# Performance work log

Hardware: AMD Instinct MI355X
Metric: run time of the kernel (lower is better)

The kernel has to match this reference:

```python
import jax, jax.numpy as jnp
import numpy as np

EPS_PD = 1e-6      # torch.nn.PairwiseDistance default eps (added to the difference)
EPS_NORM = 1e-12   # F.normalize default eps

B, D, C = 1024, 512, 256  # batch, in_features, out_features


def _l2_normalize(x, axis):
    n = jnp.linalg.norm(x, axis=axis, keepdims=True)
    return x / jnp.maximum(n, EPS_NORM)


def _pairwise_dist(a, b):
    # Faithful to torch PairwiseDistance(p=2) with the unsqueeze(2)/t().unsqueeze(0)
    # broadcast trick: norm over the feature dim of (a[:, :, None] - b.T[None, :, :] + eps).
    # a: [N, D], b: [M, D] -> [N, M]
    diff = a[:, :, None] - b.T[None, :, :] + EPS_PD  # [N, D, M]
    return jnp.sqrt(jnp.sum(diff * diff, axis=1))


def setup_inputs() -> dict:
    key = jax.random.key(0)
    k1, k2, k3 = jax.random.split(key, 3)
    return {
        "features": jax.random.normal(k1, (B, D), dtype=jnp.float32),
        "weights": jax.random.normal(k2, (C, D), dtype=jnp.float32),          # nn.init.normal_(0,1)
        "distance_scale": jax.random.normal(k3, (1,), dtype=jnp.float32),
        "use_distance_scale": 1,
    }


def reference(features, weights, distance_scale, use_distance_scale):
    f = _l2_normalize(features, axis=1)   # [B, D]
    w = _l2_normalize(weights, axis=1)    # [C, D]
    distances = _pairwise_dist(f, w)          # [B, C]
    distances_protoc = _pairwise_dist(w, w)   # [C, C]
    logits = distances - distances_protoc.sum() * 0.1
    if use_distance_scale:
        return -logits * jnp.abs(distance_scale)
    return -logits
```

## Files before the change

kernel.cpp:

```cpp
#include <hip/hip_runtime.h>
#include <math.h>

#define DIMS 512
#define BATCH 1024
#define CLS 256
#define ROWS (BATCH + CLS)

#define EPS_PD 1e-6f
#define DEPS2 (512.0f * 1e-6f * 1e-6f)
#define EPS_NORM 1e-12f

typedef short bf16x8 __attribute__((ext_vector_type(8)));
typedef float f32x4 __attribute__((ext_vector_type(4)));

__device__ __forceinline__ float waveReduceSum(float v) {
#pragma unroll
  for (int off = 32; off > 0; off >>= 1)
    v += __shfl_xor(v, off, 64);
  return v;
}

__device__ __forceinline__ unsigned short f2bf(float x) {
  unsigned int u = __float_as_uint(x);
  u += 0x7fffu + ((u >> 16) & 1u);
  return (unsigned short)(u >> 16);
}

__global__ __launch_bounds__(256) void k_norm(
    const float* __restrict__ feat, const float* __restrict__ wt,
    unsigned short* __restrict__ fnw, float* __restrict__ Srow) {
  const int r = blockIdx.x * 4 + (threadIdx.x >> 6);
  const int lane = threadIdx.x & 63;
  const float* src = (r < BATCH) ? (feat + (size_t)r * DIMS)
                                 : (wt + (size_t)(r - BATCH) * DIMS);
  const float4* s4 = (const float4*)src;

  float4 a = s4[lane];
  float4 c = s4[lane + 64];

  float ss = a.x*a.x + a.y*a.y + a.z*a.z + a.w*a.w
           + c.x*c.x + c.y*c.y + c.z*c.z + c.w*c.w;
  float sm = a.x + a.y + a.z + a.w + c.x + c.y + c.z + c.w;
  ss = waveReduceSum(ss);
  sm = waveReduceSum(sm);
  const float rn = 1.f / fmaxf(sqrtf(ss), EPS_NORM);

  ushort4 pa, pc;
  pa.x = f2bf(a.x * rn); pa.y = f2bf(a.y * rn);
  pa.z = f2bf(a.z * rn); pa.w = f2bf(a.w * rn);
  pc.x = f2bf(c.x * rn); pc.y = f2bf(c.y * rn);
  pc.z = f2bf(c.z * rn); pc.w = f2bf(c.w * rn);

  ushort4* dst = (ushort4*)(fnw + (size_t)r * DIMS);
  dst[lane] = pa;
  dst[lane + 64] = pc;

  if (lane == 0) Srow[r] = sm * rn;
}

__global__ __launch_bounds__(64) void k_protoc(
    const unsigned short* __restrict__ fnw, const float* __restrict__ Srow,
    float* __restrict__ partial) {
  const int lane = threadIdx.x;
  const int i0 = blockIdx.y * 32;
  const int j0 = blockIdx.x * 32;

  const int lm = lane & 15;
  const int lk = (lane >> 4) * 8;

  const unsigned short* arow0 = fnw + (size_t)(BATCH + i0 + lm) * DIMS + lk;
  const unsigned short* arow1 = fnw + (size_t)(BATCH + i0 + 16 + lm) * DIMS + lk;
  const unsigned short* brow0 = fnw + (size_t)(BATCH + j0 + lm) * DIMS + lk;
  const unsigned short* brow1 = fnw + (size_t)(BATCH + j0 + 16 + lm) * DIMS + lk;

  f32x4 acc00 = {0.f,0.f,0.f,0.f}, acc01 = {0.f,0.f,0.f,0.f};
  f32x4 acc10 = {0.f,0.f,0.f,0.f}, acc11 = {0.f,0.f,0.f,0.f};

#pragma unroll
  for (int k0 = 0; k0 < DIMS; k0 += 32) {
    const bf16x8 a0 = *(const bf16x8*)(arow0 + k0);
    const bf16x8 a1 = *(const bf16x8*)(arow1 + k0);
    const bf16x8 b0 = *(const bf16x8*)(brow0 + k0);
    const bf16x8 b1 = *(const bf16x8*)(brow1 + k0);
    acc00 = __builtin_amdgcn_mfma_f32_16x16x32_bf16(a0, b0, acc00, 0, 0, 0);
    acc01 = __builtin_amdgcn_mfma_f32_16x16x32_bf16(a0, b1, acc01, 0, 0, 0);
    acc10 = __builtin_amdgcn_mfma_f32_16x16x32_bf16(a1, b0, acc10, 0, 0, 0);
    acc11 = __builtin_amdgcn_mfma_f32_16x16x32_bf16(a1, b1, acc11, 0, 0, 0);
  }

  const int crow = (lane >> 4) * 4;
  const int ccol = lane & 15;

  const float swj0 = Srow[BATCH + j0 + ccol];
  const float swj1 = Srow[BATCH + j0 + 16 + ccol];

  float s = 0.f;
  const f32x4 accs[4] = {acc00, acc01, acc10, acc11};
#pragma unroll
  for (int hi = 0; hi < 2; ++hi) {
#pragma unroll
    for (int q = 0; q < 4; ++q) {
      const int i = i0 + hi * 16 + crow + q;
      const float swi = Srow[BATCH + i];
#pragma unroll
      for (int hj = 0; hj < 2; ++hj) {
        const int j = j0 + hj * 16 + ccol;
        const float dot = accs[hi * 2 + hj][q];
        const float swj = hj ? swj1 : swj0;
        float dist;
        if (i == j) {
          dist = sqrtf(DEPS2);
        } else {
          const float d2 = 2.f - 2.f * dot + 2.f * EPS_PD * (swi - swj) + DEPS2;
          dist = sqrtf(fmaxf(d2, 0.f));
        }
        s += dist;
      }
    }
  }

  s = waveReduceSum(s);
  if (lane == 0) partial[blockIdx.y * 8 + blockIdx.x] = s;
}

__global__ __launch_bounds__(64) void k_main(
    const unsigned short* __restrict__ fnw, const float* __restrict__ Srow,
    const float* __restrict__ partial, const float* __restrict__ dscale,
    const int* __restrict__ use_ds, float* __restrict__ out) {
  const int lane = threadIdx.x;
  const int r0 = blockIdx.x * 32;
  const int j0 = blockIdx.y * 32;

  const float myPartial = partial[lane];

  const int lm = lane & 15;
  const int lk = (lane >> 4) * 8;

  const unsigned short* arow0 = fnw + (size_t)(r0 + lm) * DIMS + lk;
  const unsigned short* arow1 = fnw + (size_t)(r0 + 16 + lm) * DIMS + lk;
  const unsigned short* brow0 = fnw + (size_t)(BATCH + j0 + lm) * DIMS + lk;
  const unsigned short* brow1 = fnw + (size_t)(BATCH + j0 + 16 + lm) * DIMS + lk;

  f32x4 acc00 = {0.f,0.f,0.f,0.f}, acc01 = {0.f,0.f,0.f,0.f};
  f32x4 acc10 = {0.f,0.f,0.f,0.f}, acc11 = {0.f,0.f,0.f,0.f};

#pragma unroll
  for (int k0 = 0; k0 < DIMS; k0 += 32) {
    const bf16x8 a0 = *(const bf16x8*)(arow0 + k0);
    const bf16x8 a1 = *(const bf16x8*)(arow1 + k0);
    const bf16x8 b0 = *(const bf16x8*)(brow0 + k0);
    const bf16x8 b1 = *(const bf16x8*)(brow1 + k0);
    acc00 = __builtin_amdgcn_mfma_f32_16x16x32_bf16(a0, b0, acc00, 0, 0, 0);
    acc01 = __builtin_amdgcn_mfma_f32_16x16x32_bf16(a0, b1, acc01, 0, 0, 0);
    acc10 = __builtin_amdgcn_mfma_f32_16x16x32_bf16(a1, b0, acc10, 0, 0, 0);
    acc11 = __builtin_amdgcn_mfma_f32_16x16x32_bf16(a1, b1, acc11, 0, 0, 0);
  }

  const float S = waveReduceSum(myPartial);
  const float Ssc = 0.1f * S;
  const float sc = (use_ds[0] != 0) ? fabsf(dscale[0]) : 1.0f;

  const int crow = (lane >> 4) * 4;
  const int ccol = lane & 15;

  const float swj0 = Srow[BATCH + j0 + ccol];
  const float swj1 = Srow[BATCH + j0 + 16 + ccol];

  const f32x4 accs[4] = {acc00, acc01, acc10, acc11};
#pragma unroll
  for (int hi = 0; hi < 2; ++hi) {
#pragma unroll
    for (int q = 0; q < 4; ++q) {
      const int i = r0 + hi * 16 + crow + q;
      const float sfi = Srow[i];
#pragma unroll
      for (int hj = 0; hj < 2; ++hj) {
        const int j = j0 + hj * 16 + ccol;
        const float dot = accs[hi * 2 + hj][q];
        const float swj = hj ? swj1 : swj0;
        const float d2 = 2.f - 2.f * dot + 2.f * EPS_PD * (sfi - swj) + DEPS2;
        const float dist = sqrtf(fmaxf(d2, 0.f));
        out[(size_t)i * CLS + j] = (Ssc - dist) * sc;
      }
    }
  }
}

extern "C" void kernel_launch(void* const* d_in, const int* in_sizes, int n_in,
                              void* d_out, int out_size, void* d_ws, size_t ws_size,
                              hipStream_t stream) {
  const float* feat = (const float*)d_in[0];
  const float* wt   = (const float*)d_in[1];
  const float* ds   = (const float*)d_in[2];
  const int*   use  = (const int*)d_in[3];
  float* out = (float*)d_out;

  unsigned short* fnw = (unsigned short*)d_ws;
  float* fbase   = (float*)((char*)d_ws + (size_t)ROWS * DIMS * 2);
  float* Srow    = fbase;
  float* partial = fbase + ROWS;

  k_norm<<<ROWS / 4, 256, 0, stream>>>(feat, wt, fnw, Srow);
  k_protoc<<<dim3(8, 8), 64, 0, stream>>>(fnw, Srow, partial);
  k_main<<<dim3(32, 8), 64, 0, stream>>>(fnw, Srow, partial, ds, use, out);
}
```

Measured before the change: 21.42 us.

## Store normalized bf16 rows in MFMA fragment order and use 4-wave blocks

The normalization kernel now writes bf16 data in a pre-swizzled layout: groups of 16 rows are interleaved so that each MFMA fragment load is one contiguous 1KB chunk read by 64 lanes. This targets the strided 16-byte loads that previously hit 16 different rows. The GEMM kernels are also regrouped into 256-thread blocks of four waves, which means fewer, larger blocks (64 instead of 256 for the main kernel). The partial-sum indexing is remapped to match, but the fewer blocks leave many CUs idle.

```diff
diff --git a/kernel.cpp b/kernel.cpp
--- a/kernel.cpp
+++ b/kernel.cpp
@@ -9,6 +9,7 @@
 #define EPS_PD 1e-6f
 #define DEPS2 (512.0f * 1e-6f * 1e-6f)
 #define EPS_NORM 1e-12f
+
 
 typedef short bf16x8 __attribute__((ext_vector_type(8)));
 typedef float f32x4 __attribute__((ext_vector_type(4)));
@@ -35,8 +36,8 @@
                                  : (wt + (size_t)(r - BATCH) * DIMS);
   const float4* s4 = (const float4*)src;
 
-  float4 a = s4[lane];
-  float4 c = s4[lane + 64];
+  float4 a = s4[lane * 2];
+  float4 c = s4[lane * 2 + 1];
 
   float ss = a.x*a.x + a.y*a.y + a.z*a.z + a.w*a.w
            + c.x*c.x + c.y*c.y + c.z*c.z + c.w*c.w;
@@ -45,50 +46,48 @@
   sm = waveReduceSum(sm);
   const float rn = 1.f / fmaxf(sqrtf(ss), EPS_NORM);
 
-  ushort4 pa, pc;
-  pa.x = f2bf(a.x * rn); pa.y = f2bf(a.y * rn);
-  pa.z = f2bf(a.z * rn); pa.w = f2bf(a.w * rn);
-  pc.x = f2bf(c.x * rn); pc.y = f2bf(c.y * rn);
-  pc.z = f2bf(c.z * rn); pc.w = f2bf(c.w * rn);
-
-  ushort4* dst = (ushort4*)(fnw + (size_t)r * DIMS);
-  dst[lane] = pa;
-  dst[lane + 64] = pc;
+  ushort4 p0, p1;
+  p0.x = f2bf(a.x * rn); p0.y = f2bf(a.y * rn);
+  p0.z = f2bf(a.z * rn); p0.w = f2bf(a.w * rn);
+  p1.x = f2bf(c.x * rn); p1.y = f2bf(c.y * rn);
+  p1.z = f2bf(c.z * rn); p1.w = f2bf(c.w * rn);
+
+  unsigned short* dst = fnw + (size_t)(r >> 4) * 8192 + (size_t)lane * 128 + (r & 15) * 8;
+  *(ushort4*)dst = p0;
+  *(ushort4*)(dst + 4) = p1;
 
   if (lane == 0) Srow[r] = sm * rn;
 }
 
-__global__ __launch_bounds__(64) void k_protoc(
+#define FRAG(g, k0) (*(const bf16x8*)(fnw + (size_t)(g) * 8192 + (k0) * 16 + (size_t)lane * 8))
+
+__global__ __launch_bounds__(256) void k_protoc(
     const unsigned short* __restrict__ fnw, const float* __restrict__ Srow,
     float* __restrict__ partial) {
-  const int lane = threadIdx.x;
-  const int i0 = blockIdx.y * 32;
-  const int j0 = blockIdx.x * 32;
-
-  const int lm = lane & 15;
-  const int lk = (lane >> 4) * 8;
-
-  const unsigned short* arow0 = fnw + (size_t)(BATCH + i0 + lm) * DIMS + lk;
-  const unsigned short* arow1 = fnw + (size_t)(BATCH + i0 + 16 + lm) * DIMS + lk;
-  const unsigned short* brow0 = fnw + (size_t)(BATCH + j0 + lm) * DIMS + lk;
-  const unsigned short* brow1 = fnw + (size_t)(BATCH + j0 + 16 + lm) * DIMS + lk;
+  const int lane = threadIdx.x & 63;
+  const int w = threadIdx.x >> 6;
+  const int i0 = blockIdx.y * 64 + (w >> 1) * 32;
+  const int j0 = blockIdx.x * 64 + (w & 1) * 32;
+
+  const int gA = (BATCH + i0) >> 4;
+  const int gB = (BATCH + j0) >> 4;
 
   f32x4 acc00 = {0.f,0.f,0.f,0.f}, acc01 = {0.f,0.f,0.f,0.f};
   f32x4 acc10 = {0.f,0.f,0.f,0.f}, acc11 = {0.f,0.f,0.f,0.f};
 
 #pragma unroll
   for (int k0 = 0; k0 < DIMS; k0 += 32) {
-    const bf16x8 a0 = *(const bf16x8*)(arow0 + k0);
-    const bf16x8 a1 = *(const bf16x8*)(arow1 + k0);
-    const bf16x8 b0 = *(const bf16x8*)(brow0 + k0);
-    const bf16x8 b1 = *(const bf16x8*)(brow1 + k0);
+    const bf16x8 a0 = FRAG(gA, k0);
+    const bf16x8 a1 = FRAG(gA + 1, k0);
+    const bf16x8 b0 = FRAG(gB, k0);
+    const bf16x8 b1 = FRAG(gB + 1, k0);
     acc00 = __builtin_amdgcn_mfma_f32_16x16x32_bf16(a0, b0, acc00, 0, 0, 0);
     acc01 = __builtin_amdgcn_mfma_f32_16x16x32_bf16(a0, b1, acc01, 0, 0, 0);
     acc10 = __builtin_amdgcn_mfma_f32_16x16x32_bf16(a1, b0, acc10, 0, 0, 0);
     acc11 = __builtin_amdgcn_mfma_f32_16x16x32_bf16(a1, b1, acc11, 0, 0, 0);
   }
 
-  const int crow = (lane >> 4) * 4;
+  const int crow = ((lane >> 4) & 3) * 4;
   const int ccol = lane & 15;
 
   const float swj0 = Srow[BATCH + j0 + ccol];
@@ -120,36 +119,32 @@
   }
 
   s = waveReduceSum(s);
-  if (lane == 0) partial[blockIdx.y * 8 + blockIdx.x] = s;
-}
-
-__global__ __launch_bounds__(64) void k_main(
+  if (lane == 0) partial[((blockIdx.y * 4 + blockIdx.x) << 2) + w] = s;
+}
+
+__global__ __launch_bounds__(256) void k_main(
     const unsigned short* __restrict__ fnw, const float* __restrict__ Srow,
     const float* __restrict__ partial, const float* __restrict__ dscale,
     const int* __restrict__ use_ds, float* __restrict__ out) {
-  const int lane = threadIdx.x;
-  const int r0 = blockIdx.x * 32;
-  const int j0 = blockIdx.y * 32;
+  const int lane = threadIdx.x & 63;
+  const int w = threadIdx.x >> 6;
+  const int r0 = blockIdx.x * 64 + (w >> 1) * 32;
+  const int j0 = blockIdx.y * 64 + (w & 1) * 32;
 
   const float myPartial = partial[lane];
 
-  const int lm = lane & 15;
-  const int lk = (lane >> 4) * 8;
-
-  const unsigned short* arow0 = fnw + (size_t)(r0 + lm) * DIMS + lk;
-  const unsigned short* arow1 = fnw + (size_t)(r0 + 16 + lm) * DIMS + lk;
-  const unsigned short* brow0 = fnw + (size_t)(BATCH + j0 + lm) * DIMS + lk;
-  const unsigned short* brow1 = fnw + (size_t)(BATCH + j0 + 16 + lm) * DIMS + lk;
+  const int gA = r0 >> 4;
+  const int gB = (BATCH + j0) >> 4;
 
   f32x4 acc00 = {0.f,0.f,0.f,0.f}, acc01 = {0.f,0.f,0.f,0.f};
   f32x4 acc10 = {0.f,0.f,0.f,0.f}, acc11 = {0.f,0.f,0.f,0.f};
 
 #pragma unroll
   for (int k0 = 0; k0 < DIMS; k0 += 32) {
-    const bf16x8 a0 = *(const bf16x8*)(arow0 + k0);
-    const bf16x8 a1 = *(const bf16x8*)(arow1 + k0);
-    const bf16x8 b0 = *(const bf16x8*)(brow0 + k0);
-    const bf16x8 b1 = *(const bf16x8*)(brow1 + k0);
+    const bf16x8 a0 = FRAG(gA, k0);
+    const bf16x8 a1 = FRAG(gA + 1, k0);
+    const bf16x8 b0 = FRAG(gB, k0);
+    const bf16x8 b1 = FRAG(gB + 1, k0);
     acc00 = __builtin_amdgcn_mfma_f32_16x16x32_bf16(a0, b0, acc00, 0, 0, 0);
     acc01 = __builtin_amdgcn_mfma_f32_16x16x32_bf16(a0, b1, acc01, 0, 0, 0);
     acc10 = __builtin_amdgcn_mfma_f32_16x16x32_bf16(a1, b0, acc10, 0, 0, 0);
@@ -160,7 +155,7 @@
   const float Ssc = 0.1f * S;
   const float sc = (use_ds[0] != 0) ? fabsf(dscale[0]) : 1.0f;
 
-  const int crow = (lane >> 4) * 4;
+  const int crow = ((lane >> 4) & 3) * 4;
   const int ccol = lane & 15;
 
   const float swj0 = Srow[BATCH + j0 + ccol];
@@ -201,6 +196,6 @@
   float* partial = fbase + ROWS;
 
   k_norm<<<ROWS / 4, 256, 0, stream>>>(feat, wt, fnw, Srow);
-  k_protoc<<<dim3(8, 8), 64, 0, stream>>>(fnw, Srow, partial);
-  k_main<<<dim3(32, 8), 64, 0, stream>>>(fnw, Srow, partial, ds, use, out);
-}
+  k_protoc<<<dim3(4, 4), 256, 0, stream>>>(fnw, Srow, partial);
+  k_main<<<dim3(16, 4), 256, 0, stream>>>(fnw, Srow, partial, ds, use, out);
+}
```

Result: slower. 22.45 us (+4.8%).

## Fuse normalization and prototype-distance kernels into one launch with on-the-fly normalization

Applied to the files above, without the earlier changes.

Merges the row-normalization kernel and the prototype pairwise-distance kernel into a single launch. The protoc blocks no longer wait for the normalized bf16 buffer: each recomputes its weight rows' norms and sums straight from the raw fp32 weights, then converts to bf16 for MFMA. This removes one kernel launch and the dependency between the two stages, at the cost of redundant fp32 weight reads and norm arithmetic in each protoc block. Normalization now uses one 64-thread block per row instead of four rows per 256-thread block.

```diff
diff --git a/kernel.cpp b/kernel.cpp
--- a/kernel.cpp
+++ b/kernel.cpp
@@ -26,82 +26,113 @@
   return (unsigned short)(u >> 16);
 }
 
-__global__ __launch_bounds__(256) void k_norm(
+__global__ __launch_bounds__(64) void k_norm_protoc(
     const float* __restrict__ feat, const float* __restrict__ wt,
-    unsigned short* __restrict__ fnw, float* __restrict__ Srow) {
-  const int r = blockIdx.x * 4 + (threadIdx.x >> 6);
-  const int lane = threadIdx.x & 63;
-  const float* src = (r < BATCH) ? (feat + (size_t)r * DIMS)
-                                 : (wt + (size_t)(r - BATCH) * DIMS);
-  const float4* s4 = (const float4*)src;
-
-  float4 a = s4[lane];
-  float4 c = s4[lane + 64];
-
-  float ss = a.x*a.x + a.y*a.y + a.z*a.z + a.w*a.w
-           + c.x*c.x + c.y*c.y + c.z*c.z + c.w*c.w;
-  float sm = a.x + a.y + a.z + a.w + c.x + c.y + c.z + c.w;
-  ss = waveReduceSum(ss);
-  sm = waveReduceSum(sm);
-  const float rn = 1.f / fmaxf(sqrtf(ss), EPS_NORM);
-
-  ushort4 pa, pc;
-  pa.x = f2bf(a.x * rn); pa.y = f2bf(a.y * rn);
-  pa.z = f2bf(a.z * rn); pa.w = f2bf(a.w * rn);
-  pc.x = f2bf(c.x * rn); pc.y = f2bf(c.y * rn);
-  pc.z = f2bf(c.z * rn); pc.w = f2bf(c.w * rn);
-
-  ushort4* dst = (ushort4*)(fnw + (size_t)r * DIMS);
-  dst[lane] = pa;
-  dst[lane + 64] = pc;
-
-  if (lane == 0) Srow[r] = sm * rn;
-}
-
-__global__ __launch_bounds__(64) void k_protoc(
-    const unsigned short* __restrict__ fnw, const float* __restrict__ Srow,
+    unsigned short* __restrict__ fnw, float* __restrict__ Srow,
     float* __restrict__ partial) {
+  const int b = blockIdx.x;
   const int lane = threadIdx.x;
-  const int i0 = blockIdx.y * 32;
-  const int j0 = blockIdx.x * 32;
-
-  const int lm = lane & 15;
-  const int lk = (lane >> 4) * 8;
-
-  const unsigned short* arow0 = fnw + (size_t)(BATCH + i0 + lm) * DIMS + lk;
-  const unsigned short* arow1 = fnw + (size_t)(BATCH + i0 + 16 + lm) * DIMS + lk;
-  const unsigned short* brow0 = fnw + (size_t)(BATCH + j0 + lm) * DIMS + lk;
-  const unsigned short* brow1 = fnw + (size_t)(BATCH + j0 + 16 + lm) * DIMS + lk;
+
+  if (b < ROWS) {
+    const float* src = (b < BATCH) ? (feat + (size_t)b * DIMS)
+                                   : (wt + (size_t)(b - BATCH) * DIMS);
+    const float4* s4 = (const float4*)src;
+    float4 a = s4[lane];
+    float4 c = s4[lane + 64];
+
+    float ss = a.x*a.x + a.y*a.y + a.z*a.z + a.w*a.w
+             + c.x*c.x + c.y*c.y + c.z*c.z + c.w*c.w;
+    float sm = a.x + a.y + a.z + a.w + c.x + c.y + c.z + c.w;
+    ss = waveReduceSum(ss);
+    sm = waveReduceSum(sm);
+    const float rn = 1.f / fmaxf(sqrtf(ss), EPS_NORM);
+
+    ushort4 pa, pc;
+    pa.x = f2bf(a.x * rn); pa.y = f2bf(a.y * rn);
+    pa.z = f2bf(a.z * rn); pa.w = f2bf(a.w * rn);
+    pc.x = f2bf(c.x * rn); pc.y = f2bf(c.y * rn);
+    pc.z = f2bf(c.z * rn); pc.w = f2bf(c.w * rn);
+
+    ushort4* dst = (ushort4*)(fnw + (size_t)b * DIMS);
+    dst[lane] = pa;
+    dst[lane + 64] = pc;
+    if (lane == 0) Srow[b] = sm * rn;
+    return;
+  }
+
+  const int t = b - ROWS;
+  const int i0 = (t >> 3) * 32;
+  const int j0 = (t & 7) * 32;
+  const int lr = lane & 15;
+  const int ks = (lane >> 4) * 8;
+
+  const float* wr0 = wt + (size_t)(i0 + lr) * DIMS + ks;
+  const float* wr1 = wt + (size_t)(i0 + 16 + lr) * DIMS + ks;
+  const float* wr2 = wt + (size_t)(j0 + lr) * DIMS + ks;
+  const float* wr3 = wt + (size_t)(j0 + 16 + lr) * DIMS + ks;
+  const float* wr[4] = {wr0, wr1, wr2, wr3};
+
+  float ss[4] = {0.f, 0.f, 0.f, 0.f};
+  float sm[4] = {0.f, 0.f, 0.f, 0.f};
+#pragma unroll
+  for (int k0 = 0; k0 < 16; ++k0) {
+#pragma unroll
+    for (int rr = 0; rr < 4; ++rr) {
+      const float4 x = *(const float4*)(wr[rr] + k0 * 32);
+      const float4 y = *(const float4*)(wr[rr] + k0 * 32 + 4);
+      ss[rr] += x.x*x.x + x.y*x.y + x.z*x.z + x.w*x.w
+              + y.x*y.x + y.y*y.y + y.z*y.z + y.w*y.w;
+      sm[rr] += x.x + x.y + x.z + x.w + y.x + y.y + y.z + y.w;
+    }
+  }
+  float rn[4], S[4];
+#pragma unroll
+  for (int rr = 0; rr < 4; ++rr) {
+    float s2 = ss[rr];
+    s2 += __shfl_xor(s2, 16, 64);
+    s2 += __shfl_xor(s2, 32, 64);
+    float s1 = sm[rr];
+    s1 += __shfl_xor(s1, 16, 64);
+    s1 += __shfl_xor(s1, 32, 64);
+    rn[rr] = 1.f / fmaxf(sqrtf(s2), EPS_NORM);
+    S[rr] = s1 * rn[rr];
+  }
 
   f32x4 acc00 = {0.f,0.f,0.f,0.f}, acc01 = {0.f,0.f,0.f,0.f};
   f32x4 acc10 = {0.f,0.f,0.f,0.f}, acc11 = {0.f,0.f,0.f,0.f};
-
-#pragma unroll
-  for (int k0 = 0; k0 < DIMS; k0 += 32) {
-    const bf16x8 a0 = *(const bf16x8*)(arow0 + k0);
-    const bf16x8 a1 = *(const bf16x8*)(arow1 + k0);
-    const bf16x8 b0 = *(const bf16x8*)(brow0 + k0);
-    const bf16x8 b1 = *(const bf16x8*)(brow1 + k0);
-    acc00 = __builtin_amdgcn_mfma_f32_16x16x32_bf16(a0, b0, acc00, 0, 0, 0);
-    acc01 = __builtin_amdgcn_mfma_f32_16x16x32_bf16(a0, b1, acc01, 0, 0, 0);
-    acc10 = __builtin_amdgcn_mfma_f32_16x16x32_bf16(a1, b0, acc10, 0, 0, 0);
-    acc11 = __builtin_amdgcn_mfma_f32_16x16x32_bf16(a1, b1, acc11, 0, 0, 0);
+#pragma unroll
+  for (int k0 = 0; k0 < 16; ++k0) {
+    bf16x8 fr[4];
+#pragma unroll
+    for (int rr = 0; rr < 4; ++rr) {
+      const float4 x = *(const float4*)(wr[rr] + k0 * 32);
+      const float4 y = *(const float4*)(wr[rr] + k0 * 32 + 4);
+      bf16x8 f;
+      f[0] = (short)f2bf(x.x * rn[rr]); f[1] = (short)f2bf(x.y * rn[rr]);
+      f[2] = (short)f2bf(x.z * rn[rr]); f[3] = (short)f2bf(x.w * rn[rr]);
+      f[4] = (short)f2bf(y.x * rn[rr]); f[5] = (short)f2bf(y.y * rn[rr]);
+      f[6] = (short)f2bf(y.z * rn[rr]); f[7] = (short)f2bf(y.w * rn[rr]);
+      fr[rr] = f;
+    }
+    acc00 = __builtin_amdgcn_mfma_f32_16x16x32_bf16(fr[0], fr[2], acc00, 0, 0, 0);
+    acc01 = __builtin_amdgcn_mfma_f32_16x16x32_bf16(fr[0], fr[3], acc01, 0, 0, 0);
+    acc10 = __builtin_amdgcn_mfma_f32_16x16x32_bf16(fr[1], fr[2], acc10, 0, 0, 0);
+    acc11 = __builtin_amdgcn_mfma_f32_16x16x32_bf16(fr[1], fr[3], acc11, 0, 0, 0);
   }
 
   const int crow = (lane >> 4) * 4;
   const int ccol = lane & 15;
-
-  const float swj0 = Srow[BATCH + j0 + ccol];
-  const float swj1 = Srow[BATCH + j0 + 16 + ccol];
+  const float swj0 = S[2];
+  const float swj1 = S[3];
+  const f32x4 accs[4] = {acc00, acc01, acc10, acc11};
 
   float s = 0.f;
-  const f32x4 accs[4] = {acc00, acc01, acc10, acc11};
 #pragma unroll
   for (int hi = 0; hi < 2; ++hi) {
 #pragma unroll
     for (int q = 0; q < 4; ++q) {
       const int i = i0 + hi * 16 + crow + q;
-      const float swi = Srow[BATCH + i];
+      const float swi = __shfl(hi ? S[1] : S[0], crow + q, 64);
 #pragma unroll
       for (int hj = 0; hj < 2; ++hj) {
         const int j = j0 + hj * 16 + ccol;
@@ -118,9 +149,8 @@
       }
     }
   }
-
   s = waveReduceSum(s);
-  if (lane == 0) partial[blockIdx.y * 8 + blockIdx.x] = s;
+  if (lane == 0) partial[t] = s;
 }
 
 __global__ __launch_bounds__(64) void k_main(
@@ -156,17 +186,16 @@
     acc11 = __builtin_amdgcn_mfma_f32_16x16x32_bf16(a1, b1, acc11, 0, 0, 0);
   }
 
-  const float S = waveReduceSum(myPartial);
-  const float Ssc = 0.1f * S;
+  const float Sg = waveReduceSum(myPartial);
+  const float Ssc = 0.1f * Sg;
   const float sc = (use_ds[0] != 0) ? fabsf(dscale[0]) : 1.0f;
 
   const int crow = (lane >> 4) * 4;
   const int ccol = lane & 15;
-
   const float swj0 = Srow[BATCH + j0 + ccol];
   const float swj1 = Srow[BATCH + j0 + 16 + ccol];
-
   const f32x4 accs[4] = {acc00, acc01, acc10, acc11};
+
 #pragma unroll
   for (int hi = 0; hi < 2; ++hi) {
 #pragma unroll
@@ -200,7 +229,6 @@
   float* Srow    = fbase;
   float* partial = fbase + ROWS;
 
-  k_norm<<<ROWS / 4, 256, 0, stream>>>(feat, wt, fnw, Srow);
-  k_protoc<<<dim3(8, 8), 64, 0, stream>>>(fnw, Srow, partial);
+  k_norm_protoc<<<ROWS + 64, 64, 0, stream>>>(feat, wt, fnw, Srow, partial);
   k_main<<<dim3(32, 8), 64, 0, stream>>>(fnw, Srow, partial, ds, use, out);
 }
```

After: 34.65 us. +61.8%, slower.
